# Optimization experiments

Hardware: AMD Instinct MI355X
Metric: run time of the kernel (lower is better)

Reference implementation:

```python
import jax, jax.numpy as jnp
import numpy as np

EPS = 1e-5
N_HEADS = 16

def _bn(x, g, b, m, v):
    # x: (N,C,L); inference-mode batchnorm with running stats
    scale = g * jax.lax.rsqrt(v + EPS)
    return (x - m[None, :, None]) * scale[None, :, None] + b[None, :, None]

def _conv1d(x, w, b, pad):
    # x: (N,C,L), w: (O,I,K) torch layout
    y = jax.lax.conv_general_dilated(x, w, window_strides=(1,), padding=[(pad, pad)],
                                     dimension_numbers=('NCH', 'OIH', 'NCH'))
    return y + b[None, :, None]

def _instance_norm(x):
    m = x.mean(-1, keepdims=True)
    v = x.var(-1, keepdims=True)
    return (x - m) * jax.lax.rsqrt(v + EPS)

def setup_inputs() -> dict:
    key = jax.random.key(0)
    ks = jax.random.split(key, 12)
    C, MID, N, L = 1024, 1024, 4, 1024
    s = 0.02
    d = {
        'x': jax.random.normal(ks[0], (N, C, L), jnp.float32),
        'norm_g': jnp.ones((C,), jnp.float32) + 0.1 * jax.random.normal(ks[1], (C,)),
        'norm_b': 0.1 * jax.random.normal(ks[2], (C,)),
        'norm_m': 0.05 * jax.random.normal(ks[3], (C,)),
        'norm_v': jnp.ones((C,), jnp.float32),
        'wq': s * jax.random.normal(ks[4], (C, C)),
        'wk': s * jax.random.normal(ks[5], (C, C)),
        'wv': s * jax.random.normal(ks[6], (C, C)),
        'wo': s * jax.random.normal(ks[7], (C, C)),
        'cw1': s * jax.random.normal(ks[8], (MID, C, 1)),
        'cb1': jnp.zeros((MID,), jnp.float32),
        'cw2': s * jax.random.normal(ks[9], (MID, MID, 3)),
        'cb2': jnp.zeros((MID,), jnp.float32),
        'cw3': s * jax.random.normal(ks[10], (C, MID, 1)),
        'cb3': jnp.zeros((C,), jnp.float32),
    }
    for i, cdim in [(1, MID), (2, MID), (3, C)]:
        kk = jax.random.split(ks[11], 8)
        d[f'bn{i}_g'] = jnp.ones((cdim,), jnp.float32) + 0.1 * jax.random.normal(kk[2 * i - 2], (cdim,))
        d[f'bn{i}_b'] = 0.1 * jax.random.normal(kk[2 * i - 1], (cdim,))
        d[f'bn{i}_m'] = 0.05 * jax.random.normal(jax.random.fold_in(key, 100 + i), (cdim,))
        d[f'bn{i}_v'] = jnp.ones((cdim,), jnp.float32)
    return d

def _attention(h, wq, wk, wv, wo):
    # h: (N,L,C) ; torch Linear: y = x @ W.T
    N, L, C = h.shape
    dh = C // N_HEADS
    q = (h @ wq.T).reshape(N, L, N_HEADS, dh)
    k = (h @ wk.T).reshape(N, L, N_HEADS, dh)
    v = (h @ wv.T).reshape(N, L, N_HEADS, dh)
    att = jnp.einsum('nqhd,nkhd->nhqk', q, k) / jnp.sqrt(jnp.float32(C))  # note: /sqrt(d_model) as in source
    att = jax.nn.softmax(att, axis=-1)
    o = jnp.einsum('nhqk,nkhd->nqhd', att, v).reshape(N, L, C)
    return o @ wo.T

def _forward(x, norm_g, norm_b, norm_m, norm_v, wq, wk, wv, wo,
             cw1, cb1, bn1_g, bn1_b, bn1_m, bn1_v,
             cw2, cb2, bn2_g, bn2_b, bn2_m, bn2_v,
             cw3, cb3, bn3_g, bn3_b, bn3_m, bn3_v):
    # self-attention branch (dropout is identity in eval)
    h = _bn(x, norm_g, norm_b, norm_m, norm_v).transpose(0, 2, 1)  # (N,L,C)
    h = h + _attention(h, wq, wk, wv, wo)
    h = h.transpose(0, 2, 1)  # (N,C,L)
    # IbnNet (bottleneck conv block + residual + optional InstanceNorm)
    y = jax.nn.relu(_bn(_conv1d(h, cw1, cb1, 0), bn1_g, bn1_b, bn1_m, bn1_v))
    y = jax.nn.relu(_bn(_conv1d(y, cw2, cb2, 1), bn2_g, bn2_b, bn2_m, bn2_v))
    y = _bn(_conv1d(y, cw3, cb3, 0), bn3_g, bn3_b, bn3_m, bn3_v)
    y = jax.nn.relu(_instance_norm(y + h))
    # max_pool1d(kernel=2, stride=2)
    N, C, L = y.shape
    return y.reshape(N, C, L // 2, 2).max(axis=-1)

def reference(x, norm_g, norm_b, norm_m, norm_v, wq, wk, wv, wo,
              cw1, cb1, bn1_g, bn1_b, bn1_m, bn1_v,
              cw2, cb2, bn2_g, bn2_b, bn2_m, bn2_v,
              cw3, cb3, bn3_g, bn3_b, bn3_m, bn3_v):
    return _forward(x, norm_g, norm_b, norm_m, norm_v, wq, wk, wv, wo,
                    cw1, cb1, bn1_g, bn1_b, bn1_m, bn1_v,
                    cw2, cb2, bn2_g, bn2_b, bn2_m, bn2_v,
                    cw3, cb3, bn3_g, bn3_b, bn3_m, bn3_v)
```

## Files before the change

kernel.cpp:

```cpp
#include <hip/hip_runtime.h>
#include <cstdint>
#include <cstddef>


typedef __bf16 bf16_t;
typedef __attribute__((ext_vector_type(8))) __bf16 bf16x8;
typedef __attribute__((ext_vector_type(4))) __bf16 bf16x4;
typedef __attribute__((ext_vector_type(4))) float f32x4;
typedef __attribute__((ext_vector_type(8))) unsigned short u16x8;
typedef __attribute__((address_space(1))) unsigned int gu32;
typedef __attribute__((address_space(3))) unsigned int lu32;

#define EPSF 1e-5f

__device__ __forceinline__ void glds16(const void* g, void* l) {
  __builtin_amdgcn_global_load_lds((gu32*)g, (lu32*)l, 16, 0, 0);
}

__device__ __forceinline__ f32x4 mfma16(bf16x8 a, bf16x8 b, f32x4 c) {
  return __builtin_amdgcn_mfma_f32_16x16x32_bf16(a, b, c, 0, 0, 0);
}

__global__ void bn_consts_k(const float* __restrict__ g, const float* __restrict__ b,
                            const float* __restrict__ m, const float* __restrict__ v,
                            const float* __restrict__ cb,
                            float* __restrict__ sc, float* __restrict__ sh, int C) {
  int i = blockIdx.x * 256 + threadIdx.x;
  if (i < C) {
    float s = g[i] * rsqrtf(v[i] + EPSF);
    sc[i] = s;
    sh[i] = b[i] + ((cb ? cb[i] : 0.f) - m[i]) * s;
  }
}

__global__ __launch_bounds__(256)
void bn_transpose_k(const float* __restrict__ x, const float* __restrict__ sc,
                    const float* __restrict__ sh, bf16_t* __restrict__ H0b) {
  __shared__ float T[32][33];
  const int n = blockIdx.x, c0 = blockIdx.y * 32, l0 = blockIdx.z * 32;
  const int tx = threadIdx.x & 31, ty = threadIdx.x >> 5;
#pragma unroll
  for (int cc = 0; cc < 4; ++cc) {
    int c = c0 + ty + cc * 8;
    float v = x[((size_t)(n * 1024 + c) << 10) + l0 + tx];
    T[ty + cc * 8][tx] = v * sc[c] + sh[c];
  }
  __syncthreads();
#pragma unroll
  for (int cc = 0; cc < 4; ++cc) {
    int l = l0 + ty + cc * 8;
    float v = T[tx][ty + cc * 8];
    H0b[((size_t)(n * 1024 + l) << 10) + c0 + tx] = (bf16_t)v;
  }
}

__global__ void cast6_k(const float* __restrict__ s0, const float* __restrict__ s1,
                        const float* __restrict__ s2, const float* __restrict__ s3,
                        const float* __restrict__ s4, const float* __restrict__ s5,
                        bf16_t* __restrict__ d0, bf16_t* __restrict__ d1,
                        bf16_t* __restrict__ d2, bf16_t* __restrict__ d3,
                        bf16_t* __restrict__ d4, bf16_t* __restrict__ d5) {
  const int b = blockIdx.x, which = b >> 10;
  const int i = (b & 1023) * 256 + threadIdx.x;
  const float* s; bf16_t* d;
  switch (which) {
    case 0: s = s0; d = d0; break;
    case 1: s = s1; d = d1; break;
    case 2: s = s2; d = d2; break;
    case 3: s = s3; d = d3; break;
    case 4: s = s4; d = d4; break;
    default: s = s5; d = d5; break;
  }
  f32x4 v = *(const f32x4*)(s + (size_t)i * 4);
  bf16x4 o;
  o[0] = (bf16_t)v[0]; o[1] = (bf16_t)v[1]; o[2] = (bf16_t)v[2]; o[3] = (bf16_t)v[3];
  *(bf16x4*)(d + (size_t)i * 4) = o;
}

__global__ void pack_w2_k(const float* __restrict__ s, bf16_t* __restrict__ d) {
  int i = blockIdx.x * 256 + threadIdx.x;
  int o = i / 3072;
  int r = i - o * 3072;
  int c = r / 3;
  int k = r - c * 3;
  d[(size_t)o * 3072 + k * 1024 + c] = (bf16_t)s[i];
}

__global__ void zero_a2_edges_k(bf16_t* __restrict__ A2) {
  int i = blockIdx.x * 256 + threadIdx.x;
  int n = i >> 11, r = (i >> 10) & 1, c = i & 1023;
  size_t row = (size_t)(n * 1024 + (r ? 1023 : 0));
  A2[row * 3072 + (r ? 2048 : 0) + c] = (bf16_t)0.f;
}

__global__ __launch_bounds__(256)
void gemm_nt(const bf16_t* __restrict__ A, const bf16_t* __restrict__ B, int K,
             int nNT, int qkv, float alpha, const float* __restrict__ bnScale,
             const float* __restrict__ bnShift, int doRelu,
             const float* __restrict__ resid, const bf16_t* __restrict__ residB,
             float* __restrict__ outF, bf16_t* __restrict__ outB,
             bf16_t* __restrict__ outA2) {
  __shared__ __align__(16) bf16_t As[2][128 * 64];
  __shared__ __align__(16) bf16_t Bs[2][64 * 64];

  const int bid = blockIdx.x;
  const int wg = (bid & 7) * (gridDim.x >> 3) + (bid >> 3);
  const int mt = wg / nNT, nt = wg - mt * nNT;
  const int tileM = mt * 128, tileN = nt * 64;

  const int tid = threadIdx.x;
  const int lane = tid & 63;
  const int w = tid >> 6, wr = w >> 1, wc = w & 1;
  const int l16 = lane & 15, g = lane >> 4;

  const bf16_t* aSrc[4];
  const bf16_t* bSrc[2];
#pragma unroll
  for (int it = 0; it < 4; ++it) {
    int q = it * 256 + tid, r = q >> 3, s = q & 7;
    aSrc[it] = A + (size_t)(tileM + r) * K + ((s ^ (r & 7)) * 8);
  }
#pragma unroll
  for (int it = 0; it < 2; ++it) {
    int q = it * 256 + tid, r = q >> 3, s = q & 7;
    bSrc[it] = B + (size_t)(tileN + r) * K + ((s ^ (r & 7)) * 8);
  }

  f32x4 acc[4][2];
#pragma unroll
  for (int m = 0; m < 4; ++m)
#pragma unroll
    for (int n = 0; n < 2; ++n) acc[m][n] = {0.f, 0.f, 0.f, 0.f};

#pragma unroll
  for (int it = 0; it < 4; ++it) glds16(aSrc[it], &As[0][(it * 256 + tid) * 8]);
#pragma unroll
  for (int it = 0; it < 2; ++it) glds16(bSrc[it], &Bs[0][(it * 256 + tid) * 8]);
  __syncthreads();

  int buf = 0;
  for (int k0 = 0; k0 < K; k0 += 64) {
    if (k0 + 64 < K) {
#pragma unroll
      for (int it = 0; it < 4; ++it)
        glds16(aSrc[it] + k0 + 64, &As[buf ^ 1][(it * 256 + tid) * 8]);
#pragma unroll
      for (int it = 0; it < 2; ++it)
        glds16(bSrc[it] + k0 + 64, &Bs[buf ^ 1][(it * 256 + tid) * 8]);
    }
#pragma unroll
    for (int kk = 0; kk < 2; ++kk) {
      bf16x8 af[4], bfr[2];
#pragma unroll
      for (int m = 0; m < 4; ++m) {
        int r = wr * 64 + m * 16 + l16;
        af[m] = *(const bf16x8*)(&As[buf][r * 64 + (((kk * 4 + g) ^ (r & 7)) * 8)]);
      }
#pragma unroll
      for (int n = 0; n < 2; ++n) {
        int r = wc * 32 + n * 16 + l16;
        bfr[n] = *(const bf16x8*)(&Bs[buf][r * 64 + (((kk * 4 + g) ^ (r & 7)) * 8)]);
      }
#pragma unroll
      for (int m = 0; m < 4; ++m)
#pragma unroll
        for (int n = 0; n < 2; ++n) acc[m][n] = mfma16(af[m], bfr[n], acc[m][n]);
    }
    __syncthreads();
    buf ^= 1;
  }

#pragma unroll
  for (int m = 0; m < 4; ++m) {
#pragma unroll
    for (int n = 0; n < 2; ++n) {
#pragma unroll
      for (int j = 0; j < 4; ++j) {
        const int gr = tileM + wr * 64 + m * 16 + g * 4 + j;
        const int gc = tileN + wc * 32 + n * 16 + l16;
        if (qkv) {
          const int which = gc >> 10, c = gc & 1023;
          float v = acc[m][n][j] * (which == 0 ? 0.03125f : 1.f);
          if (which == 2)
            outB[8388608 + ((size_t)(gr >> 10) << 20) + ((size_t)c << 10) + (gr & 1023)] =
                (bf16_t)v;
          else
            outB[(size_t)which * 4194304 + ((size_t)gr << 10) + c] = (bf16_t)v;
        } else {
          float v = acc[m][n][j] * alpha;
          if (bnScale) v = v * bnScale[gc] + bnShift[gc];
          if (resid) v += resid[((size_t)gr << 10) + gc];
          if (residB) v += (float)residB[((size_t)gr << 10) + gc];
          if (doRelu) v = fmaxf(v, 0.f);
          if (outF) outF[((size_t)gr << 10) + gc] = v;
          if (outB) outB[((size_t)gr << 10) + gc] = (bf16_t)v;
          if (outA2) {
            const int l = gr & 1023;
            const bf16_t bv = (bf16_t)v;
            outA2[(size_t)gr * 3072 + 1024 + gc] = bv;
            if (l < 1023) outA2[(size_t)(gr + 1) * 3072 + gc] = bv;
            if (l > 0) outA2[(size_t)(gr - 1) * 3072 + 2048 + gc] = bv;
          }
        }
      }
    }
  }
}

__global__ __launch_bounds__(256)
void attn_fwd(const bf16_t* __restrict__ Qb, const bf16_t* __restrict__ Kb,
              const bf16_t* __restrict__ Vt, bf16_t* __restrict__ AO) {
  __shared__ __align__(16) bf16_t Ks[2][64][64];
  __shared__ __align__(16) bf16_t Vs[2][64][64];
  __shared__ __align__(16) bf16_t Ps[4][2][16][64];

  const int bid = blockIdx.x;
  const int xcd = bid & 7, idx = bid >> 3;
  const int head = xcd * 8 + (idx >> 3);
  const int qblk = idx & 7;
  const int n = head >> 4, h = head & 15;

  const int tid = threadIdx.x, lane = tid & 63, w = tid >> 6;
  const int l16 = lane & 15, g = lane >> 4;
  const int qbase = qblk * 128 + w * 32;

  bf16x8 aq[2][2];
#pragma unroll
  for (int s = 0; s < 2; ++s) {
    const size_t qoff = ((size_t)(n * 1024 + qbase + s * 16 + l16) << 10) + h * 64;
    aq[s][0] = *(const bf16x8*)(Qb + qoff + g * 8);
    aq[s][1] = *(const bf16x8*)(Qb + qoff + 32 + g * 8);
  }

  const bf16_t* Khead = Kb + ((size_t)(n * 1024) << 10) + h * 64;
  const bf16_t* Vhead = Vt + ((size_t)n << 20) + ((size_t)(h * 64) << 10);

  f32x4 oa[2][4];
  float psum[2][4];
#pragma unroll
  for (int s = 0; s < 2; ++s)
#pragma unroll
    for (int i = 0; i < 4; ++i) {
      oa[s][i] = {0.f, 0.f, 0.f, 0.f};
      psum[s][i] = 0.f;
    }

#pragma unroll
  for (int it = 0; it < 2; ++it) {
    int q = it * 256 + tid, r = q >> 3, c = q & 7;
    glds16(Khead + ((size_t)r << 10) + ((c ^ (r & 7)) * 8), &Ks[0][r][c * 8]);
    glds16(Vhead + ((size_t)r << 10) + ((c ^ (r & 7)) * 8), &Vs[0][r][c * 8]);
  }
  asm volatile("s_waitcnt vmcnt(0)" ::: "memory");
  __syncthreads();

  int buf = 0;
  for (int t = 0; t < 16; ++t) {
    if (t < 15) {
      const int kv0 = (t + 1) * 64;
#pragma unroll
      for (int it = 0; it < 2; ++it) {
        int q = it * 256 + tid, r = q >> 3, c = q & 7;
        glds16(Khead + ((size_t)(kv0 + r) << 10) + ((c ^ (r & 7)) * 8),
               &Ks[buf ^ 1][r][c * 8]);
        glds16(Vhead + ((size_t)r << 10) + kv0 + ((c ^ (r & 7)) * 8),
               &Vs[buf ^ 1][r][c * 8]);
      }
    }
    bf16x8 kf[8];
#pragma unroll
    for (int nf = 0; nf < 4; ++nf) {
      const int r = nf * 16 + l16;
      kf[2 * nf]     = *(const bf16x8*)(&Ks[buf][r][((g)     ^ (r & 7)) * 8]);
      kf[2 * nf + 1] = *(const bf16x8*)(&Ks[buf][r][((4 + g) ^ (r & 7)) * 8]);
    }
#pragma unroll
    for (int s = 0; s < 2; ++s) {
      f32x4 sc[4];
#pragma unroll
      for (int nf = 0; nf < 4; ++nf) sc[nf] = {0.f, 0.f, 0.f, 0.f};
#pragma unroll
      for (int nf = 0; nf < 4; ++nf) {
        sc[nf] = mfma16(aq[s][0], kf[2 * nf], sc[nf]);
        sc[nf] = mfma16(aq[s][1], kf[2 * nf + 1], sc[nf]);
      }
#pragma unroll
      for (int nf = 0; nf < 4; ++nf)
#pragma unroll
        for (int j = 0; j < 4; ++j) {
          float p = __expf(sc[nf][j]);
          psum[s][j] += p;
          const int row = g * 4 + j;
          const int ch = (nf * 2 + (l16 >> 3)) ^ (row & 7);
          Ps[w][s][row][ch * 8 + (l16 & 7)] = (bf16_t)p;
        }
    }
    bf16x8 vf[8];
#pragma unroll
    for (int nf = 0; nf < 4; ++nf) {
      const int r = nf * 16 + l16;
      vf[2 * nf]     = *(const bf16x8*)(&Vs[buf][r][((g)     ^ (r & 7)) * 8]);
      vf[2 * nf + 1] = *(const bf16x8*)(&Vs[buf][r][((4 + g) ^ (r & 7)) * 8]);
    }
#pragma unroll
    for (int s = 0; s < 2; ++s)
#pragma unroll
      for (int kk = 0; kk < 2; ++kk) {
        const int ch = (kk * 4 + g) ^ (l16 & 7);
        bf16x8 pa = *(const bf16x8*)(&Ps[w][s][l16][ch * 8]);
#pragma unroll
        for (int nf = 0; nf < 4; ++nf)
          oa[s][nf] = mfma16(pa, vf[2 * nf + kk], oa[s][nf]);
      }
    asm volatile("s_waitcnt vmcnt(0)" ::: "memory");
    __syncthreads();
    buf ^= 1;
  }

#pragma unroll
  for (int s = 0; s < 2; ++s)
#pragma unroll
    for (int j = 0; j < 4; ++j) {
      float sv = psum[s][j];
#pragma unroll
      for (int o = 1; o < 16; o <<= 1) sv += __shfl_xor(sv, o);
      psum[s][j] = sv;
    }
#pragma unroll
  for (int s = 0; s < 2; ++s)
#pragma unroll
    for (int nf = 0; nf < 4; ++nf)
#pragma unroll
      for (int j = 0; j < 4; ++j) {
        const int q = qbase + s * 16 + g * 4 + j;
        AO[((size_t)(n * 1024 + q) << 10) + h * 64 + nf * 16 + l16] =
            (bf16_t)(oa[s][nf][j] / psum[s][j]);
      }
}

__global__ void in_stats_k(const float* __restrict__ Z, float* __restrict__ ps,
                           float* __restrict__ pq) {
  const int n = blockIdx.x, c = blockIdx.y * 256 + threadIdx.x, z = blockIdx.z;
  float s = 0.f, s2 = 0.f;
  for (int i = 0; i < 128; ++i) {
    float v = Z[((size_t)(n * 1024 + z * 128 + i) << 10) + c];
    s += v;
    s2 += v * v;
  }
  ps[z * 4096 + n * 1024 + c] = s;
  pq[z * 4096 + n * 1024 + c] = s2;
}

__global__ __launch_bounds__(256)
void finalize_k(const float* __restrict__ Z, const float* __restrict__ ps,
                const float* __restrict__ pq, float* __restrict__ out) {
  __shared__ float T[32][33];
  const int n = blockIdx.x, c0 = blockIdx.y * 32, j0 = blockIdx.z * 32;
  const int tx = threadIdx.x & 31, ty = threadIdx.x >> 5;
  const int c = c0 + tx;
  float s = 0.f, q = 0.f;
#pragma unroll
  for (int z = 0; z < 8; ++z) {
    s += ps[z * 4096 + n * 1024 + c];
    q += pq[z * 4096 + n * 1024 + c];
  }
  const float mean = s * (1.f / 1024.f);
  const float var = q * (1.f / 1024.f) - mean * mean;
  const float rstd = rsqrtf(var + EPSF);
#pragma unroll
  for (int jj = 0; jj < 4; ++jj) {
    const int j = j0 + ty + jj * 8;
    float a = Z[((size_t)(n * 1024 + 2 * j) << 10) + c];
    float b = Z[((size_t)(n * 1024 + 2 * j + 1) << 10) + c];
    float v = (fmaxf(a, b) - mean) * rstd;
    T[ty + jj * 8][tx] = fmaxf(v, 0.f);
  }
  __syncthreads();
#pragma unroll
  for (int jj = 0; jj < 4; ++jj)
    out[((size_t)(n * 1024 + c0 + ty + jj * 8) << 9) + j0 + tx] = T[tx][ty + jj * 8];
}

extern "C" void kernel_launch(void* const* d_in, const int* in_sizes, int n_in,
                              void* d_out, int out_size, void* d_ws, size_t ws_size,
                              hipStream_t stream) {
  const float* x      = (const float*)d_in[0];
  const float* norm_g = (const float*)d_in[1];
  const float* norm_b = (const float*)d_in[2];
  const float* norm_m = (const float*)d_in[3];
  const float* norm_v = (const float*)d_in[4];
  const float* wq     = (const float*)d_in[5];
  const float* wk     = (const float*)d_in[6];
  const float* wv     = (const float*)d_in[7];
  const float* wo     = (const float*)d_in[8];
  const float* cw1    = (const float*)d_in[9];
  const float* cb1    = (const float*)d_in[10];
  const float* cw2    = (const float*)d_in[11];
  const float* cb2    = (const float*)d_in[12];
  const float* cw3    = (const float*)d_in[13];
  const float* cb3    = (const float*)d_in[14];
  const float* bn1_g  = (const float*)d_in[15];
  const float* bn1_b  = (const float*)d_in[16];
  const float* bn1_m  = (const float*)d_in[17];
  const float* bn1_v  = (const float*)d_in[18];
  const float* bn2_g  = (const float*)d_in[19];
  const float* bn2_b  = (const float*)d_in[20];
  const float* bn2_m  = (const float*)d_in[21];
  const float* bn2_v  = (const float*)d_in[22];
  const float* bn3_g  = (const float*)d_in[23];
  const float* bn3_b  = (const float*)d_in[24];
  const float* bn3_m  = (const float*)d_in[25];
  const float* bn3_v  = (const float*)d_in[26];

  char* ws = (char*)d_ws;
  const size_t MB = 1024 * 1024;
  float*  Zf  = (float*)(ws);
  float*  H2f = (float*)(ws + 16 * MB);
  bf16_t* H0b = (bf16_t*)(ws + 32 * MB);
  bf16_t* Y2  = H0b;
  bf16_t* Qb  = (bf16_t*)(ws + 40 * MB);
  bf16_t* Kb  = (bf16_t*)(ws + 48 * MB);
  bf16_t* Vt  = (bf16_t*)(ws + 56 * MB);
  bf16_t* A2  = Qb;
  bf16_t* H2b = (bf16_t*)(ws + 72 * MB);
  bf16_t* AOb = (bf16_t*)(ws + 64 * MB);
  bf16_t* wqb = (bf16_t*)(ws + 80 * MB);
  bf16_t* wkb = (bf16_t*)(ws + 82 * MB);
  bf16_t* wvb = (bf16_t*)(ws + 84 * MB);
  bf16_t* wob = (bf16_t*)(ws + 86 * MB);
  bf16_t* w1b = (bf16_t*)(ws + 88 * MB);
  bf16_t* w3b = (bf16_t*)(ws + 90 * MB);
  bf16_t* w2b = (bf16_t*)(ws + 92 * MB);
  float* sc0 = (float*)(ws + 98 * MB);
  float* sh0 = sc0 + 1024;
  float* sc1 = sc0 + 2048;
  float* sh1 = sc0 + 3072;
  float* sc2 = sc0 + 4096;
  float* sh2 = sc0 + 5120;
  float* sc3 = sc0 + 6144;
  float* sh3 = sc0 + 7168;
  float* ps  = sc0 + 8192;
  float* pq  = ps + 32768;

  bn_consts_k<<<4, 256, 0, stream>>>(norm_g, norm_b, norm_m, norm_v, nullptr, sc0, sh0, 1024);
  bn_consts_k<<<4, 256, 0, stream>>>(bn1_g, bn1_b, bn1_m, bn1_v, cb1, sc1, sh1, 1024);
  bn_consts_k<<<4, 256, 0, stream>>>(bn2_g, bn2_b, bn2_m, bn2_v, cb2, sc2, sh2, 1024);
  bn_consts_k<<<4, 256, 0, stream>>>(bn3_g, bn3_b, bn3_m, bn3_v, cb3, sc3, sh3, 1024);

  bn_transpose_k<<<dim3(4, 32, 32), 256, 0, stream>>>(x, sc0, sh0, H0b);

  cast6_k<<<6144, 256, 0, stream>>>(wq, wk, wv, wo, cw1, cw3,
                                    wqb, wkb, wvb, wob, w1b, w3b);
  pack_w2_k<<<12288, 256, 0, stream>>>(cw2, w2b);

  gemm_nt<<<1536, 256, 0, stream>>>(H0b, wqb, 1024, 48, 1, 1.f, nullptr, nullptr, 0,
                                    nullptr, nullptr, nullptr, Qb, nullptr);

  attn_fwd<<<512, 256, 0, stream>>>(Qb, Kb, Vt, AOb);

  zero_a2_edges_k<<<32, 256, 0, stream>>>(A2);

  gemm_nt<<<512, 256, 0, stream>>>(AOb, wob, 1024, 16, 0, 1.f, nullptr, nullptr, 0,
                                   nullptr, H0b, H2f, H2b, nullptr);
  gemm_nt<<<512, 256, 0, stream>>>(H2b, w1b, 1024, 16, 0, 1.f, sc1, sh1, 1,
                                   nullptr, nullptr, nullptr, nullptr, A2);
  gemm_nt<<<512, 256, 0, stream>>>(A2, w2b, 3072, 16, 0, 1.f, sc2, sh2, 1,
                                   nullptr, nullptr, nullptr, Y2, nullptr);
  gemm_nt<<<512, 256, 0, stream>>>(Y2, w3b, 1024, 16, 0, 1.f, sc3, sh3, 0,
                                   H2f, nullptr, Zf, nullptr, nullptr);

  in_stats_k<<<dim3(4, 4, 8), 256, 0, stream>>>(Zf, ps, pq);
  finalize_k<<<dim3(4, 32, 16), 256, 0, stream>>>(Zf, ps, pq, (float*)d_out);
}
```

Before: 261.8 us.

## Replace conv im2col buffer with padded overlapping-row layout and drop fp32 intermediates

The k=3 conv input is no longer expanded into a three-times-wide im2col buffer. The first pointwise GEMM now writes into a row-padded buffer, and the conv GEMM reads each A row as three consecutive padded rows through a separate leading dimension and a padded row index. The fp32 residual and conv-output buffers are replaced by bf16: the residual now comes from H2b and Z is stored in bf16 for the instance-norm kernels. The four batchnorm-constant launches are also merged into one. This cuts global write and read traffic and launch count, at the cost of lower precision in the residual path and in the instance-norm statistics.

```diff
diff --git a/kernel.cpp b/kernel.cpp
--- a/kernel.cpp
+++ b/kernel.cpp
@@ -21,16 +21,25 @@
   return __builtin_amdgcn_mfma_f32_16x16x32_bf16(a, b, c, 0, 0, 0);
 }
 
-__global__ void bn_consts_k(const float* __restrict__ g, const float* __restrict__ b,
-                            const float* __restrict__ m, const float* __restrict__ v,
-                            const float* __restrict__ cb,
-                            float* __restrict__ sc, float* __restrict__ sh, int C) {
-  int i = blockIdx.x * 256 + threadIdx.x;
-  if (i < C) {
-    float s = g[i] * rsqrtf(v[i] + EPSF);
-    sc[i] = s;
-    sh[i] = b[i] + ((cb ? cb[i] : 0.f) - m[i]) * s;
-  }
+struct BnAll {
+  const float *g0, *b0, *m0, *v0;
+  const float *g1, *b1, *m1, *v1, *cb1;
+  const float *g2, *b2, *m2, *v2, *cb2;
+  const float *g3, *b3, *m3, *v3, *cb3;
+};
+__global__ void bn_consts4_k(BnAll a, float* __restrict__ base) {
+  const int sec = blockIdx.x >> 2;
+  const int i = (blockIdx.x & 3) * 256 + threadIdx.x;
+  const float *g, *b, *m, *v, *cb;
+  switch (sec) {
+    case 0: g = a.g0; b = a.b0; m = a.m0; v = a.v0; cb = nullptr; break;
+    case 1: g = a.g1; b = a.b1; m = a.m1; v = a.v1; cb = a.cb1; break;
+    case 2: g = a.g2; b = a.b2; m = a.m2; v = a.v2; cb = a.cb2; break;
+    default: g = a.g3; b = a.b3; m = a.m3; v = a.v3; cb = a.cb3; break;
+  }
+  float s = g[i] * rsqrtf(v[i] + EPSF);
+  base[sec * 2048 + i] = s;
+  base[sec * 2048 + 1024 + i] = b[i] + ((cb ? cb[i] : 0.f) - m[i]) * s;
 }
 
 __global__ __launch_bounds__(256)
@@ -86,20 +95,18 @@
   d[(size_t)o * 3072 + k * 1024 + c] = (bf16_t)s[i];
 }
 
-__global__ void zero_a2_edges_k(bf16_t* __restrict__ A2) {
+__global__ void zero_y1p_pads_k(bf16_t* __restrict__ Y1p) {
   int i = blockIdx.x * 256 + threadIdx.x;
   int n = i >> 11, r = (i >> 10) & 1, c = i & 1023;
-  size_t row = (size_t)(n * 1024 + (r ? 1023 : 0));
-  A2[row * 3072 + (r ? 2048 : 0) + c] = (bf16_t)0.f;
+  Y1p[(size_t)(n * 1026 + (r ? 1025 : 0)) * 1024 + c] = (bf16_t)0.f;
 }
 
 __global__ __launch_bounds__(256)
 void gemm_nt(const bf16_t* __restrict__ A, const bf16_t* __restrict__ B, int K,
-             int nNT, int qkv, float alpha, const float* __restrict__ bnScale,
-             const float* __restrict__ bnShift, int doRelu,
-             const float* __restrict__ resid, const bf16_t* __restrict__ residB,
-             float* __restrict__ outF, bf16_t* __restrict__ outB,
-             bf16_t* __restrict__ outA2) {
+             int lda, int ldb, int aPad, int outPad, int nNT, int qkv,
+             const float* __restrict__ bnScale, const float* __restrict__ bnShift,
+             int doRelu, const bf16_t* __restrict__ residB,
+             bf16_t* __restrict__ outB) {
   __shared__ __align__(16) bf16_t As[2][128 * 64];
   __shared__ __align__(16) bf16_t Bs[2][64 * 64];
 
@@ -118,12 +125,14 @@
 #pragma unroll
   for (int it = 0; it < 4; ++it) {
     int q = it * 256 + tid, r = q >> 3, s = q & 7;
-    aSrc[it] = A + (size_t)(tileM + r) * K + ((s ^ (r & 7)) * 8);
+    int ar = tileM + r;
+    if (aPad) ar = (ar >> 10) * 1026 + (ar & 1023);
+    aSrc[it] = A + (size_t)ar * lda + ((s ^ (r & 7)) * 8);
   }
 #pragma unroll
   for (int it = 0; it < 2; ++it) {
     int q = it * 256 + tid, r = q >> 3, s = q & 7;
-    bSrc[it] = B + (size_t)(tileN + r) * K + ((s ^ (r & 7)) * 8);
+    bSrc[it] = B + (size_t)(tileN + r) * ldb + ((s ^ (r & 7)) * 8);
   }
 
   f32x4 acc[4][2];
@@ -187,20 +196,13 @@
           else
             outB[(size_t)which * 4194304 + ((size_t)gr << 10) + c] = (bf16_t)v;
         } else {
-          float v = acc[m][n][j] * alpha;
+          float v = acc[m][n][j];
           if (bnScale) v = v * bnScale[gc] + bnShift[gc];
-          if (resid) v += resid[((size_t)gr << 10) + gc];
           if (residB) v += (float)residB[((size_t)gr << 10) + gc];
           if (doRelu) v = fmaxf(v, 0.f);
-          if (outF) outF[((size_t)gr << 10) + gc] = v;
-          if (outB) outB[((size_t)gr << 10) + gc] = (bf16_t)v;
-          if (outA2) {
-            const int l = gr & 1023;
-            const bf16_t bv = (bf16_t)v;
-            outA2[(size_t)gr * 3072 + 1024 + gc] = bv;
-            if (l < 1023) outA2[(size_t)(gr + 1) * 3072 + gc] = bv;
-            if (l > 0) outA2[(size_t)(gr - 1) * 3072 + 2048 + gc] = bv;
-          }
+          size_t orow = gr;
+          if (outPad) orow = (size_t)((gr >> 10) * 1026 + (gr & 1023) + 1);
+          outB[orow * 1024 + gc] = (bf16_t)v;
         }
       }
     }
@@ -338,12 +340,12 @@
       }
 }
 
-__global__ void in_stats_k(const float* __restrict__ Z, float* __restrict__ ps,
+__global__ void in_stats_k(const bf16_t* __restrict__ Z, float* __restrict__ ps,
                            float* __restrict__ pq) {
   const int n = blockIdx.x, c = blockIdx.y * 256 + threadIdx.x, z = blockIdx.z;
   float s = 0.f, s2 = 0.f;
   for (int i = 0; i < 128; ++i) {
-    float v = Z[((size_t)(n * 1024 + z * 128 + i) << 10) + c];
+    float v = (float)Z[((size_t)(n * 1024 + z * 128 + i) << 10) + c];
     s += v;
     s2 += v * v;
   }
@@ -352,7 +354,7 @@
 }
 
 __global__ __launch_bounds__(256)
-void finalize_k(const float* __restrict__ Z, const float* __restrict__ ps,
+void finalize_k(const bf16_t* __restrict__ Z, const float* __restrict__ ps,
                 const float* __restrict__ pq, float* __restrict__ out) {
   __shared__ float T[32][33];
   const int n = blockIdx.x, c0 = blockIdx.y * 32, j0 = blockIdx.z * 32;
@@ -370,8 +372,8 @@
 #pragma unroll
   for (int jj = 0; jj < 4; ++jj) {
     const int j = j0 + ty + jj * 8;
-    float a = Z[((size_t)(n * 1024 + 2 * j) << 10) + c];
-    float b = Z[((size_t)(n * 1024 + 2 * j + 1) << 10) + c];
+    float a = (float)Z[((size_t)(n * 1024 + 2 * j) << 10) + c];
+    float b = (float)Z[((size_t)(n * 1024 + 2 * j + 1) << 10) + c];
     float v = (fmaxf(a, b) - mean) * rstd;
     T[ty + jj * 8][tx] = fmaxf(v, 0.f);
   }
@@ -414,16 +416,15 @@
 
   char* ws = (char*)d_ws;
   const size_t MB = 1024 * 1024;
-  float*  Zf  = (float*)(ws);
-  float*  H2f = (float*)(ws + 16 * MB);
+  bf16_t* Zb  = (bf16_t*)(ws);
   bf16_t* H0b = (bf16_t*)(ws + 32 * MB);
   bf16_t* Y2  = H0b;
   bf16_t* Qb  = (bf16_t*)(ws + 40 * MB);
   bf16_t* Kb  = (bf16_t*)(ws + 48 * MB);
   bf16_t* Vt  = (bf16_t*)(ws + 56 * MB);
-  bf16_t* A2  = Qb;
+  bf16_t* Y1p = Qb;
+  bf16_t* AOb = (bf16_t*)(ws + 64 * MB);
   bf16_t* H2b = (bf16_t*)(ws + 72 * MB);
-  bf16_t* AOb = (bf16_t*)(ws + 64 * MB);
   bf16_t* wqb = (bf16_t*)(ws + 80 * MB);
   bf16_t* wkb = (bf16_t*)(ws + 82 * MB);
   bf16_t* wvb = (bf16_t*)(ws + 84 * MB);
@@ -431,21 +432,19 @@
   bf16_t* w1b = (bf16_t*)(ws + 88 * MB);
   bf16_t* w3b = (bf16_t*)(ws + 90 * MB);
   bf16_t* w2b = (bf16_t*)(ws + 92 * MB);
-  float* sc0 = (float*)(ws + 98 * MB);
-  float* sh0 = sc0 + 1024;
-  float* sc1 = sc0 + 2048;
-  float* sh1 = sc0 + 3072;
-  float* sc2 = sc0 + 4096;
-  float* sh2 = sc0 + 5120;
-  float* sc3 = sc0 + 6144;
-  float* sh3 = sc0 + 7168;
-  float* ps  = sc0 + 8192;
+  float* cb   = (float*)(ws + 98 * MB);
+  float* sc0 = cb,        * sh0 = cb + 1024;
+  float* sc1 = cb + 2048, * sh1 = cb + 3072;
+  float* sc2 = cb + 4096, * sh2 = cb + 5120;
+  float* sc3 = cb + 6144, * sh3 = cb + 7168;
+  float* ps  = cb + 8192;
   float* pq  = ps + 32768;
 
-  bn_consts_k<<<4, 256, 0, stream>>>(norm_g, norm_b, norm_m, norm_v, nullptr, sc0, sh0, 1024);
-  bn_consts_k<<<4, 256, 0, stream>>>(bn1_g, bn1_b, bn1_m, bn1_v, cb1, sc1, sh1, 1024);
-  bn_consts_k<<<4, 256, 0, stream>>>(bn2_g, bn2_b, bn2_m, bn2_v, cb2, sc2, sh2, 1024);
-  bn_consts_k<<<4, 256, 0, stream>>>(bn3_g, bn3_b, bn3_m, bn3_v, cb3, sc3, sh3, 1024);
+  BnAll ba = {norm_g, norm_b, norm_m, norm_v,
+              bn1_g, bn1_b, bn1_m, bn1_v, cb1,
+              bn2_g, bn2_b, bn2_m, bn2_v, cb2,
+              bn3_g, bn3_b, bn3_m, bn3_v, cb3};
+  bn_consts4_k<<<16, 256, 0, stream>>>(ba, cb);
 
   bn_transpose_k<<<dim3(4, 32, 32), 256, 0, stream>>>(x, sc0, sh0, H0b);
 
@@ -453,22 +452,22 @@
                                     wqb, wkb, wvb, wob, w1b, w3b);
   pack_w2_k<<<12288, 256, 0, stream>>>(cw2, w2b);
 
-  gemm_nt<<<1536, 256, 0, stream>>>(H0b, wqb, 1024, 48, 1, 1.f, nullptr, nullptr, 0,
-                                    nullptr, nullptr, nullptr, Qb, nullptr);
+  gemm_nt<<<1536, 256, 0, stream>>>(H0b, wqb, 1024, 1024, 1024, 0, 0, 48, 1,
+                                    nullptr, nullptr, 0, nullptr, Qb);
 
   attn_fwd<<<512, 256, 0, stream>>>(Qb, Kb, Vt, AOb);
 
-  zero_a2_edges_k<<<32, 256, 0, stream>>>(A2);
-
-  gemm_nt<<<512, 256, 0, stream>>>(AOb, wob, 1024, 16, 0, 1.f, nullptr, nullptr, 0,
-                                   nullptr, H0b, H2f, H2b, nullptr);
-  gemm_nt<<<512, 256, 0, stream>>>(H2b, w1b, 1024, 16, 0, 1.f, sc1, sh1, 1,
-                                   nullptr, nullptr, nullptr, nullptr, A2);
-  gemm_nt<<<512, 256, 0, stream>>>(A2, w2b, 3072, 16, 0, 1.f, sc2, sh2, 1,
-                                   nullptr, nullptr, nullptr, Y2, nullptr);
-  gemm_nt<<<512, 256, 0, stream>>>(Y2, w3b, 1024, 16, 0, 1.f, sc3, sh3, 0,
-                                   H2f, nullptr, Zf, nullptr, nullptr);
-
-  in_stats_k<<<dim3(4, 4, 8), 256, 0, stream>>>(Zf, ps, pq);
-  finalize_k<<<dim3(4, 32, 16), 256, 0, stream>>>(Zf, ps, pq, (float*)d_out);
-}
+  zero_y1p_pads_k<<<32, 256, 0, stream>>>(Y1p);
+
+  gemm_nt<<<512, 256, 0, stream>>>(AOb, wob, 1024, 1024, 1024, 0, 0, 16, 0,
+                                   nullptr, nullptr, 0, H0b, H2b);
+  gemm_nt<<<512, 256, 0, stream>>>(H2b, w1b, 1024, 1024, 1024, 0, 1, 16, 0,
+                                   sc1, sh1, 1, nullptr, Y1p);
+  gemm_nt<<<512, 256, 0, stream>>>(Y1p, w2b, 3072, 1024, 3072, 1, 0, 16, 0,
+                                   sc2, sh2, 1, nullptr, Y2);
+  gemm_nt<<<512, 256, 0, stream>>>(Y2, w3b, 1024, 1024, 1024, 0, 0, 16, 0,
+                                   sc3, sh3, 0, H2b, Zb);
+
+  in_stats_k<<<dim3(4, 4, 8), 256, 0, stream>>>(Zb, ps, pq);
+  finalize_k<<<dim3(4, 32, 16), 256, 0, stream>>>(Zb, ps, pq, (float*)d_out);
+}
```

After: 253.2 us. 3.3% less time.
